# Kernel optimization log

Hardware: AMD Instinct MI355X
Metric: run time of the kernel (lower is better)

## Reference

```python
import jax, jax.numpy as jnp
import numpy as np

VOCAB = 90000
MAX_ID = 95000
EFFECT_DIM = 758
ADD_DIM = 10
EMBED_DIM = 768  # EFFECT_DIM + ADD_DIM
CTX = 1024
MAX_SYN = 8


def setup_inputs() -> dict:
    key = jax.random.key(0)
    k_ids, k_emb, k_rev, k_tab, k_msk = jax.random.split(key, 5)
    ids = jax.random.randint(k_ids, (CTX,), 0, VOCAB, dtype=jnp.int64)
    W_emb = jax.random.normal(k_emb, (MAX_ID, EFFECT_DIM), dtype=jnp.float32)
    W_rev = jax.random.normal(k_rev, (EMBED_DIM, MAX_ID), dtype=jnp.float32)
    padding = 0.1 * jnp.ones((CTX, ADD_DIM), dtype=jnp.float32)
    # synonym ids live in [VOCAB, MAX_ID); only some slots are active (variable-length lists)
    syn_table = jax.random.randint(k_tab, (MAX_ID, MAX_SYN), VOCAB, MAX_ID, dtype=jnp.int32)
    syn_mask = jax.random.randint(k_msk, (MAX_ID, MAX_SYN), 0, 2, dtype=jnp.int32)
    # tokens >= VOCAB (synonym ids themselves) have no synonyms
    syn_mask = syn_mask.at[VOCAB:].set(0)
    return {"ids": ids, "W_emb": W_emb, "W_rev": W_rev, "padding": padding,
            "syn_table": syn_table, "syn_mask": syn_mask}


def reference(ids, W_emb, W_rev, padding, syn_table, syn_mask):
    # VirtualEmbedding: base gather + masked synonym gather/scale/accumulate.
    # i_sum is computed BEFORE the synonym loop in the original, so each
    # synonym contribution is independent -> vectorized masked reduction.
    # (Dropout in eval mode is the identity.)
    base = W_emb[ids]                              # [L, D]
    syn_ids = syn_table[ids]                       # [L, K]
    syn = W_emb[syn_ids]                           # [L, K, D]
    mask = syn_mask[ids].astype(base.dtype)        # [L, K]
    i_sum = jnp.sum(base, axis=-1, keepdims=True)  # [L, 1]
    s_sum = jnp.sum(syn, axis=-1)                  # [L, K]
    d = i_sum / s_sum                              # [L, K]
    emb = base + jnp.einsum('lk,lkd->ld', mask * d, syn)
    # concat fixed context padding, then ReverseEmbedding projection to vocab
    full = jnp.concatenate([emb, padding], axis=1)  # [L, EMBED_DIM]
    return full @ W_rev                             # [L, MAX_ID]
```

## Files before the change

kernel.cpp:

```cpp
#include <hip/hip_runtime.h>
#include <stdint.h>

#define EFFECT_DIM 758
#define ADD_DIM 10
#define EMBED_DIM 768
#define NCOLS 95000
#define NSYN 8
#define NROWS 1024
#define TILE_B 32768
#define NT64 1485
#define NWG (2 * NT64)

typedef __attribute__((ext_vector_type(8))) __bf16 bf16x8;
typedef __attribute__((ext_vector_type(16))) float f32x16;
typedef __attribute__((ext_vector_type(4))) uint32_t u32x4;


static __device__ __forceinline__ uint32_t pack2(float a, float b) {
  uint32_t r;
  asm("v_cvt_pk_bf16_f32 %0, %1, %2" : "=v"(r) : "v"(a), "v"(b));
  return r;
}

#define F4C(f, i) ((i) == 0 ? (f).x : (i) == 1 ? (f).y : (i) == 2 ? (f).z : (f).w)

__global__ __launch_bounds__(256) void emb_kernel(
    const int* __restrict__ ids, const float* __restrict__ W_emb,
    const float* __restrict__ padding, const int* __restrict__ syn_table,
    const int* __restrict__ syn_mask, char* __restrict__ ws)
{
  const int l = blockIdx.x;
  const int t = threadIdx.x;
  const int id = ids[l];
  int sid[NSYN];
  int msk[NSYN];
#pragma unroll
  for (int k = 0; k < NSYN; ++k) {
    sid[k] = syn_table[id * NSYN + k];
    msk[k] = syn_mask[id * NSYN + k];
  }

  double p[9] = {0, 0, 0, 0, 0, 0, 0, 0, 0};
  for (int d = t; d < EFFECT_DIM; d += 256) {
    p[0] += (double)W_emb[(size_t)id * EFFECT_DIM + d];
#pragma unroll
    for (int k = 0; k < NSYN; ++k)
      p[k + 1] += (double)W_emb[(size_t)sid[k] * EFFECT_DIM + d];
  }

  __shared__ double s_red[9][4];
  const int w = t >> 6;
#pragma unroll
  for (int k = 0; k < 9; ++k) {
    double v = p[k];
#pragma unroll
    for (int off = 32; off > 0; off >>= 1) v += __shfl_down(v, off, 64);
    if ((t & 63) == 0) s_red[k][w] = v;
  }
  __syncthreads();

  const double isum = s_red[0][0] + s_red[0][1] + s_red[0][2] + s_red[0][3];
  float coef[NSYN];
#pragma unroll
  for (int k = 0; k < NSYN; ++k) {
    double ss = s_red[k + 1][0] + s_red[k + 1][1] + s_red[k + 1][2] + s_red[k + 1][3];
    coef[k] = msk[k] ? (float)(isum / ss) : 0.0f;
  }

  const int r = l & 255;
  char* wbase = ws + (size_t)(l >> 8) * (12 * TILE_B);

  for (int j = t; j < 384; j += 256) {
    const int d0 = 2 * j;
    float v0, v1;
    if (d0 < EFFECT_DIM) {
      const float* bp = W_emb + (size_t)id * EFFECT_DIM + d0;
      v0 = bp[0];
      v1 = bp[1];
#pragma unroll
      for (int k = 0; k < NSYN; ++k) {
        const float* sp = W_emb + (size_t)sid[k] * EFFECT_DIM + d0;
        v0 = fmaf(coef[k], sp[0], v0);
        v1 = fmaf(coef[k], sp[1], v1);
      }
    } else {
      v0 = padding[l * ADD_DIM + (d0 - EFFECT_DIM)];
      v1 = padding[l * ADD_DIM + (d0 + 1 - EFFECT_DIM)];
    }
    const int ks   = j >> 5;
    const int jl   = j & 31;
    const int kk   = jl >> 3;
    const int byte = (jl & 7) * 4;
    const int lane = (r & 31) + ((byte >> 4) << 5);
    *(uint32_t*)(wbase + ks * TILE_B + kk * 8192 + (r >> 5) * 1024 +
                 lane * 16 + (byte & 15)) = pack2(v0, v1);
  }
}

__global__ __launch_bounds__(512, 2) void gemm_kres(
    const float* __restrict__ Wrev, const char* __restrict__ Abuf,
    float* __restrict__ out)
{
  __shared__ char lds[98304];
  const int t = threadIdx.x;
  const int l = t & 63;
  const int w = t >> 6;

  const int orig = blockIdx.x;
  const int xcd  = orig & 7;
  const int q = NWG / 8, rr = NWG % 8;
  const int chunk0 = (xcd < rr) ? xcd * (q + 1) : rr * (q + 1) + (xcd - rr) * q;
  const int work = chunk0 + (orig >> 3);
  const int mt = work & 1;
  const int nt = work >> 1;
  const int n0 = nt * 64;

  {
    const int kc = t >> 4;
    const int n4 = (t & 15) * 4;
    const bool valid = (n0 + n4 + 4) <= NCOLS;
#pragma unroll
    for (int rnd = 0; rnd < 3; ++rnd) {
      const int kbase = rnd * 256 + kc * 8;
      float4 v[8];
      const float* p = Wrev + (size_t)kbase * NCOLS + n0 + n4;
#pragma unroll
      for (int j = 0; j < 8; ++j)
        v[j] = valid ? *(const float4*)(p + (size_t)j * NCOLS)
                     : float4{0.0f, 0.0f, 0.0f, 0.0f};
      const int kb = kbase >> 4;
      const int kh = kc & 1;
#pragma unroll
      for (int i = 0; i < 4; ++i) {
        const int n = n4 + i;
        u32x4 u;
#pragma unroll
        for (int j2 = 0; j2 < 4; ++j2)
          u[j2] = pack2(F4C(v[2 * j2], i), F4C(v[2 * j2 + 1], i));
        *(u32x4*)(lds + kb * 2048 + (n >> 5) * 1024 +
                  ((n & 31) + (kh << 5)) * 16) = u;
      }
    }
  }
  __syncthreads();

  const int mtq0 = mt * 2 + (w >> 2);
  const int grp0 = (w & 3) * 2;
  const char* abase = Abuf + (size_t)mtq0 * (12 * TILE_B) + grp0 * 1024 + l * 16;

  f32x16 acc[2][2] = {};

  for (int ks = 0; ks < 12; ++ks) {
    const char* at = abase + ks * TILE_B;
    const char* bt = lds + ks * 8192 + l * 16;
#pragma unroll
    for (int kk = 0; kk < 4; ++kk) {
      bf16x8 a0 = *(const bf16x8*)(at + kk * 8192);
      bf16x8 a1 = *(const bf16x8*)(at + kk * 8192 + 1024);
      bf16x8 b0 = *(const bf16x8*)(bt + kk * 2048);
      bf16x8 b1 = *(const bf16x8*)(bt + kk * 2048 + 1024);
      acc[0][0] = __builtin_amdgcn_mfma_f32_32x32x16_bf16(a0, b0, acc[0][0], 0, 0, 0);
      acc[0][1] = __builtin_amdgcn_mfma_f32_32x32x16_bf16(a0, b1, acc[0][1], 0, 0, 0);
      acc[1][0] = __builtin_amdgcn_mfma_f32_32x32x16_bf16(a1, b0, acc[1][0], 0, 0, 0);
      acc[1][1] = __builtin_amdgcn_mfma_f32_32x32x16_bf16(a1, b1, acc[1][1], 0, 0, 0);
    }
  }

  const int rbase = (mtq0 * 8 + grp0) * 32 + 4 * (l >> 5);
#pragma unroll
  for (int nr = 0; nr < 2; ++nr) {
    const int gc = n0 + nr * 32 + (l & 31);
    if (gc < NCOLS) {
#pragma unroll
      for (int mr = 0; mr < 2; ++mr)
#pragma unroll
        for (int reg = 0; reg < 16; ++reg) {
          const int row = rbase + mr * 32 + (reg & 3) + 8 * (reg >> 2);
          out[(size_t)row * NCOLS + gc] = acc[mr][nr][reg];
        }
    }
  }
}

extern "C" void kernel_launch(void* const* d_in, const int* in_sizes, int n_in,
                              void* d_out, int out_size, void* d_ws, size_t ws_size,
                              hipStream_t stream) {
  const int*   ids       = (const int*)d_in[0];
  const float* W_emb     = (const float*)d_in[1];
  const float* W_rev     = (const float*)d_in[2];
  const float* padding   = (const float*)d_in[3];
  const int*   syn_table = (const int*)d_in[4];
  const int*   syn_mask  = (const int*)d_in[5];
  float* out = (float*)d_out;
  char*  ws  = (char*)d_ws;

  hipLaunchKernelGGL(emb_kernel, dim3(NROWS), dim3(256), 0, stream,
                     ids, W_emb, padding, syn_table, syn_mask, ws);

  hipLaunchKernelGGL(gemm_kres, dim3(NWG), dim3(512), 0, stream,
                     W_rev, ws, out);
}
```

Measured before the change: 346.1 us.

## Double-buffer W_rev k-slices in LDS and widen GEMM tile to 128 columns

```diff
diff --git a/kernel.cpp b/kernel.cpp
--- a/kernel.cpp
+++ b/kernel.cpp
@@ -8,8 +8,8 @@
 #define NSYN 8
 #define NROWS 1024
 #define TILE_B 32768
-#define NT64 1485
-#define NWG (2 * NT64)
+#define NTN 743
+#define NWG (2 * NTN)
 
 typedef __attribute__((ext_vector_type(8))) __bf16 bf16x8;
 typedef __attribute__((ext_vector_type(16))) float f32x16;
@@ -21,8 +21,6 @@
   asm("v_cvt_pk_bf16_f32 %0, %1, %2" : "=v"(r) : "v"(a), "v"(b));
   return r;
 }
-
-#define F4C(f, i) ((i) == 0 ? (f).x : (i) == 1 ? (f).y : (i) == 2 ? (f).z : (f).w)
 
 __global__ __launch_bounds__(256) void emb_kernel(
     const int* __restrict__ ids, const float* __restrict__ W_emb,
@@ -97,85 +95,107 @@
   }
 }
 
-__global__ __launch_bounds__(512, 2) void gemm_kres(
+__global__ __launch_bounds__(512, 2) void gemm_fused(
     const float* __restrict__ Wrev, const char* __restrict__ Abuf,
     float* __restrict__ out)
 {
-  __shared__ char lds[98304];
+  __shared__ char lds[32768];
   const int t = threadIdx.x;
   const int l = t & 63;
   const int w = t >> 6;
-
-  const int orig = blockIdx.x;
-  const int xcd  = orig & 7;
-  const int q = NWG / 8, rr = NWG % 8;
-  const int chunk0 = (xcd < rr) ? xcd * (q + 1) : rr * (q + 1) + (xcd - rr) * q;
-  const int work = chunk0 + (orig >> 3);
+  const int ms = w >> 1;
+  const int nh = w & 1;
+
+  const int orig  = blockIdx.x;
+  const int xcd   = orig & 7;
+  const int local = orig >> 3;
+  const int chunk0 = (xcd < 6) ? xcd * 186 : 6 * 186 + (xcd - 6) * 185;
+  const int work = chunk0 + local;
   const int mt = work & 1;
   const int nt = work >> 1;
-  const int n0 = nt * 64;
-
-  {
-    const int kc = t >> 4;
-    const int n4 = (t & 15) * 4;
-    const bool valid = (n0 + n4 + 4) <= NCOLS;
-#pragma unroll
-    for (int rnd = 0; rnd < 3; ++rnd) {
-      const int kbase = rnd * 256 + kc * 8;
-      float4 v[8];
-      const float* p = Wrev + (size_t)kbase * NCOLS + n0 + n4;
-#pragma unroll
-      for (int j = 0; j < 8; ++j)
-        v[j] = valid ? *(const float4*)(p + (size_t)j * NCOLS)
-                     : float4{0.0f, 0.0f, 0.0f, 0.0f};
-      const int kb = kbase >> 4;
-      const int kh = kc & 1;
-#pragma unroll
-      for (int i = 0; i < 4; ++i) {
-        const int n = n4 + i;
-        u32x4 u;
-#pragma unroll
-        for (int j2 = 0; j2 < 4; ++j2)
-          u[j2] = pack2(F4C(v[2 * j2], i), F4C(v[2 * j2 + 1], i));
-        *(u32x4*)(lds + kb * 2048 + (n >> 5) * 1024 +
-                  ((n & 31) + (kh << 5)) * 16) = u;
-      }
-    }
-  }
+  const int n0 = nt * 128;
+
+  const int sn = t & 127;
+  const int kg = t >> 7;
+  const int gn = n0 + sn;
+  const bool valid = gn < NCOLS;
+  const int swlane = sn & 31;
+  char* const bB = (char*)lds + kg * 4096 + (sn >> 5) * 1024;
+
+  float br[16];
+
+#define BLOAD(ksi)                                                        \
+  {                                                                       \
+    const float* p = Wrev + (size_t)((ksi) * 64 + kg * 16) * NCOLS + gn;  \
+    _Pragma("unroll") for (int j = 0; j < 16; ++j)                        \
+      br[j] = valid ? p[(size_t)j * NCOLS] : 0.0f;                        \
+  }
+
+#define BSTORE(buf)                                                       \
+  {                                                                       \
+    u32x4 u0, u1;                                                         \
+    _Pragma("unroll") for (int j = 0; j < 4; ++j) {                       \
+      u0[j] = pack2(br[2 * j], br[2 * j + 1]);                            \
+      u1[j] = pack2(br[8 + 2 * j], br[9 + 2 * j]);                        \
+    }                                                                     \
+    char* bb = bB + (buf) * 16384;                                        \
+    *(u32x4*)(bb + swlane * 16) = u0;                                     \
+    *(u32x4*)(bb + (swlane + 32) * 16) = u1;                              \
+  }
+
+  BLOAD(0);
+  BSTORE(0);
   __syncthreads();
 
-  const int mtq0 = mt * 2 + (w >> 2);
-  const int grp0 = (w & 3) * 2;
-  const char* abase = Abuf + (size_t)mtq0 * (12 * TILE_B) + grp0 * 1024 + l * 16;
-
-  f32x16 acc[2][2] = {};
+  const int mtq = mt * 2 + (ms >> 1);
+  const char* abase =
+      Abuf + (size_t)mtq * (12 * TILE_B) + ((ms & 1) * 4) * 1024 + l * 16;
+
+  f32x16 acc[4][2] = {};
 
   for (int ks = 0; ks < 12; ++ks) {
+    if (ks < 11) BLOAD(ks + 1);
+
     const char* at = abase + ks * TILE_B;
-    const char* bt = lds + ks * 8192 + l * 16;
+    const char* bt = (const char*)lds + (ks & 1) * 16384 + nh * 2048 + l * 16;
+
 #pragma unroll
     for (int kk = 0; kk < 4; ++kk) {
+      bf16x8 b0 = *(const bf16x8*)(bt + kk * 4096);
+      bf16x8 b1 = *(const bf16x8*)(bt + kk * 4096 + 1024);
       bf16x8 a0 = *(const bf16x8*)(at + kk * 8192);
       bf16x8 a1 = *(const bf16x8*)(at + kk * 8192 + 1024);
-      bf16x8 b0 = *(const bf16x8*)(bt + kk * 2048);
-      bf16x8 b1 = *(const bf16x8*)(bt + kk * 2048 + 1024);
+      bf16x8 a2 = *(const bf16x8*)(at + kk * 8192 + 2048);
+      bf16x8 a3 = *(const bf16x8*)(at + kk * 8192 + 3072);
+      __builtin_amdgcn_s_setprio(1);
       acc[0][0] = __builtin_amdgcn_mfma_f32_32x32x16_bf16(a0, b0, acc[0][0], 0, 0, 0);
       acc[0][1] = __builtin_amdgcn_mfma_f32_32x32x16_bf16(a0, b1, acc[0][1], 0, 0, 0);
       acc[1][0] = __builtin_amdgcn_mfma_f32_32x32x16_bf16(a1, b0, acc[1][0], 0, 0, 0);
       acc[1][1] = __builtin_amdgcn_mfma_f32_32x32x16_bf16(a1, b1, acc[1][1], 0, 0, 0);
+      acc[2][0] = __builtin_amdgcn_mfma_f32_32x32x16_bf16(a2, b0, acc[2][0], 0, 0, 0);
+      acc[2][1] = __builtin_amdgcn_mfma_f32_32x32x16_bf16(a2, b1, acc[2][1], 0, 0, 0);
+      acc[3][0] = __builtin_amdgcn_mfma_f32_32x32x16_bf16(a3, b0, acc[3][0], 0, 0, 0);
+      acc[3][1] = __builtin_amdgcn_mfma_f32_32x32x16_bf16(a3, b1, acc[3][1], 0, 0, 0);
+      __builtin_amdgcn_s_setprio(0);
     }
-  }
-
-  const int rbase = (mtq0 * 8 + grp0) * 32 + 4 * (l >> 5);
+
+    if (ks < 11) BSTORE((ks + 1) & 1);
+    __syncthreads();
+  }
+#undef BLOAD
+#undef BSTORE
+
+  const int lh = l >> 5;
 #pragma unroll
   for (int nr = 0; nr < 2; ++nr) {
-    const int gc = n0 + nr * 32 + (l & 31);
+    const int gc = n0 + (nh * 2 + nr) * 32 + (l & 31);
     if (gc < NCOLS) {
 #pragma unroll
-      for (int mr = 0; mr < 2; ++mr)
+      for (int mr = 0; mr < 4; ++mr)
 #pragma unroll
         for (int reg = 0; reg < 16; ++reg) {
-          const int row = rbase + mr * 32 + (reg & 3) + 8 * (reg >> 2);
+          const int row = mt * 512 + ms * 128 + mr * 32 +
+                          (reg & 3) + 8 * (reg >> 2) + 4 * lh;
           out[(size_t)row * NCOLS + gc] = acc[mr][nr][reg];
         }
     }
@@ -197,6 +217,6 @@
   hipLaunchKernelGGL(emb_kernel, dim3(NROWS), dim3(256), 0, stream,
                      ids, W_emb, padding, syn_table, syn_mask, ws);
 
-  hipLaunchKernelGGL(gemm_kres, dim3(NWG), dim3(512), 0, stream,
+  hipLaunchKernelGGL(gemm_fused, dim3(NWG), dim3(512), 0, stream,
                      W_rev, ws, out);
 }
```

After: 352.3 us. Within noise of the previous version (+1.8%).
